# Kernel optimization log

Hardware: AMD Instinct MI355X
Metric: run time of the kernel (lower is better)

Reference implementation:

```python
import jax, jax.numpy as jnp
import numpy as np

IN_FF = 7  # joints
MASK = np.ones(9, dtype=np.float32)  # [P(3), RPY sin/cos (6)]


def _mlp(x, params):
    # params: list of (W, b); sigmoid after every layer except the last (predict)
    h = x
    for W, b in params[:-1]:
        h = jax.nn.sigmoid(h @ W + b)
    W, b = params[-1]
    return h @ W + b


def _rpy_head(x, params):
    # FeedForwardNet_RPY forward: y -> [sin(y0), cos(y1)], angle = atan2(sin, cos)
    y = _mlp(x, params)
    s = jnp.sin(y[..., 0])
    c = jnp.cos(y[..., 1])
    ang = jnp.arctan2(s, c)
    return jnp.stack([s, c, ang], axis=-1)  # (..., 3)


def setup_inputs():
    key = jax.random.key(0)
    ks = jax.random.split(key, 26)
    m = 16384
    d = {"x": jax.random.normal(ks[0], (m, 2 * IN_FF), jnp.float32)}

    def lin(k, fi, fo, name, i):
        k1, k2 = jax.random.split(k)
        lim = 1.0 / np.sqrt(fi)  # torch Linear default init
        d[name + "_W" + str(i)] = jax.random.uniform(k1, (fi, fo), jnp.float32, -lim, lim)
        d[name + "_b" + str(i)] = jax.random.uniform(k2, (fo,), jnp.float32, -lim, lim)

    idx = 1
    for name, dims in [("pos", [7, 512, 512, 3]), ("roll", [7, 256, 256, 2]),
                       ("pitch", [7, 256, 256, 2]), ("yaw", [7, 256, 256, 2])]:
        for i in range(3):
            lin(ks[idx], dims[i], dims[i + 1], name, i)
            idx += 1
    return d


def _forward(x, pos_p, roll_p, pitch_p, yaw_p):
    mask = jnp.asarray(MASK)
    M_P, M_RPY = mask[:3], mask[3:]
    q, qdot = x[:, :IN_FF], x[:, IN_FF:]

    # position net: forward + per-sample Jacobian (exact, replaces the autograd loop)
    P = _mlp(q, pos_p)                                          # (m, 3)
    J_P = jax.vmap(jax.jacfwd(lambda z: _mlp(z, pos_p)))(q)     # (m, 3, 7)
    vel = jnp.einsum("moi,mi->mo", J_P, qdot)                   # bmm(J_P, jointVels)
    P = P * M_P
    vel = vel * M_P

    heads = []
    for p in (roll_p, pitch_p, yaw_p):
        f = lambda z, p=p: _rpy_head(z, p)
        y = f(q)                                # (m, 3): [sin, cos, angle]
        J = jax.vmap(jax.jacfwd(f))(q)          # (m, 3, 7)
        v = jnp.einsum("moi,mi->mo", J[:, :2, :], qdot)  # (m, 2)
        heads.append((y, J, v))
    (yR, JR, vR), (yPi, JPi, vPi), (yY, JY, vY) = heads

    # order: [roll_sin, pitch_sin, yaw_sin, roll_cos, pitch_cos, yaw_cos]
    RPY = jnp.stack([yR[:, 0], yPi[:, 0], yY[:, 0], yR[:, 1], yPi[:, 1], yY[:, 1]], axis=1) * M_RPY
    vel_RPY = jnp.stack([vR[:, 0], vPi[:, 0], vY[:, 0], vR[:, 1], vPi[:, 1], vY[:, 1]], axis=1) * M_RPY
    J_RPY = jnp.stack([JR[:, 0], JPi[:, 0], JY[:, 0], JR[:, 1], JPi[:, 1], JY[:, 1]], axis=1)  # (m,6,7)

    out = jnp.concatenate([P, RPY, vel, vel_RPY], axis=1)            # (m, 18)
    J_tot = jnp.concatenate([J_P, J_RPY], axis=1)                    # (m, 9, 7)
    out_angles = jnp.concatenate([P, yR[:, 2:3], yPi[:, 2:3], yY[:, 2:3]], axis=1)       # (m, 6)
    J_tot_angles = jnp.concatenate([J_P, JR[:, 2:3], JPi[:, 2:3], JY[:, 2:3]], axis=1)   # (m, 6, 7)
    return out, J_tot, out_angles, J_tot_angles


def reference(x, pos_W0, pos_b0, pos_W1, pos_b1, pos_W2, pos_b2,
              roll_W0, roll_b0, roll_W1, roll_b1, roll_W2, roll_b2,
              pitch_W0, pitch_b0, pitch_W1, pitch_b1, pitch_W2, pitch_b2,
              yaw_W0, yaw_b0, yaw_W1, yaw_b1, yaw_W2, yaw_b2):
    pos_p = [(pos_W0, pos_b0), (pos_W1, pos_b1), (pos_W2, pos_b2)]
    roll_p = [(roll_W0, roll_b0), (roll_W1, roll_b1), (roll_W2, roll_b2)]
    pitch_p = [(pitch_W0, pitch_b0), (pitch_W1, pitch_b1), (pitch_W2, pitch_b2)]
    yaw_p = [(yaw_W0, yaw_b0), (yaw_W1, yaw_b1), (yaw_W2, yaw_b2)]
    return _forward(x, pos_p, roll_p, pitch_p, yaw_p)
```

## Files before the change

kernel.cpp:

```cpp
#include <hip/hip_runtime.h>
#include <math.h>

typedef __attribute__((ext_vector_type(8))) short short8;
typedef __attribute__((ext_vector_type(4))) float floatx4;

__device__ __forceinline__ float sig(float z) { return 1.0f / (1.0f + __expf(-z)); }

__device__ __forceinline__ unsigned short f2bf(float f) {
    unsigned u = __float_as_uint(f);
    u = (u + 0x7FFFu + ((u >> 16) & 1u)) >> 16;
    return (unsigned short)u;
}

__global__ void convert_w1(const float* __restrict__ src, unsigned short* __restrict__ dst,
                           int H, int logH) {
    int idx = blockIdx.x * 256 + threadIdx.x;
    if (idx >= H * H) return;
    int n = idx & (H - 1), k = idx >> logH;
    int KT = H >> 5;
    int blk = (n >> 4) * KT + (k >> 5);
    int lane = ((k >> 3) & 3) * 16 + (n & 15);
    int j = k & 7;
    dst[(blk * 64 + lane) * 8 + j] = f2bf(src[idx]);
}

struct PosS {
    float B0[512], B1[512], W2[1536];
    float Q[8][8], Qd[8][8];
    float Acc[4][64][3], Sum[64][3];
};
struct RpyS {
    float B0[256], B1[256], W2[512];
    float Q[16][8], Qd[16][8];
    float Acc[4][128][2], Sum[128][2];
};

__global__ __launch_bounds__(256, 2)
void fused_mfma(const float* __restrict__ x,
                const float* __restrict__ pW0, const float* __restrict__ pb0,
                const float* __restrict__ pb1,
                const float* __restrict__ pW2, const float* __restrict__ pb2,
                const float* __restrict__ rW0_, const float* __restrict__ rb0_,
                const float* __restrict__ rb1_,
                const float* __restrict__ rW2_, const float* __restrict__ rb2_,
                const float* __restrict__ piW0, const float* __restrict__ pib0,
                const float* __restrict__ pib1,
                const float* __restrict__ piW2, const float* __restrict__ pib2,
                const float* __restrict__ yW0, const float* __restrict__ yb0,
                const float* __restrict__ yb1,
                const float* __restrict__ yW2, const float* __restrict__ yb2,
                const unsigned short* __restrict__ wsBase,
                float* __restrict__ out, int ns)
{
    extern __shared__ unsigned short sA[];
    __shared__ union { PosS p; RpyS r; } sU;

    const int tid = threadIdx.x;
    const int f = blockIdx.x;
    const int g = f / 5, r5 = f % 5;
    const size_t JTOT = (size_t)ns * 18, OUTA = (size_t)ns * 81, JANG = (size_t)ns * 87;
    const floatx4 z4 = {0.f, 0.f, 0.f, 0.f};
    const int w = tid >> 6, lane = tid & 63;
    const int quad = lane >> 4, col = lane & 15;
    const int srcl = lane & 47;

    if (r5 < 2) {
        const int m0 = (g * 2 + r5) * 8;
        const unsigned short* wsW1 = wsBase;

        for (int i = tid; i < 512;  i += 256) { sU.p.B0[i] = pb0[i]; sU.p.B1[i] = pb1[i]; }
        for (int i = tid; i < 1536; i += 256) sU.p.W2[i] = pW2[i];
        if (tid < 112) {
            int m = tid / 14, c = tid % 14;
            float v = x[(m0 + m) * 14 + c];
            if (c < 7) sU.p.Q[m][c] = v; else sU.p.Qd[m][c - 7] = v;
        }
        __syncthreads();

        const float4* W04 = (const float4*)pW0;
        #pragma unroll
        for (int t = 0; t < 2; ++t) {
            int item = tid + t * 256;
            int s = item >> 6, k8 = item & 63;
            float q[7], w0v[7][8];
            #pragma unroll
            for (int i = 0; i < 7; i++) {
                q[i] = sU.p.Q[s][i];
                float4 a = W04[i * 128 + k8 * 2], b4 = W04[i * 128 + k8 * 2 + 1];
                w0v[i][0]=a.x; w0v[i][1]=a.y; w0v[i][2]=a.z; w0v[i][3]=a.w;
                w0v[i][4]=b4.x; w0v[i][5]=b4.y; w0v[i][6]=b4.z; w0v[i][7]=b4.w;
            }
            float hv[8], dv[8];
            #pragma unroll
            for (int jj = 0; jj < 8; jj++) {
                float z = sU.p.B0[k8 * 8 + jj];
                #pragma unroll
                for (int i = 0; i < 7; i++) z = fmaf(q[i], w0v[i][jj], z);
                float h = sig(z);
                hv[jj] = h; dv[jj] = h - h * h;
            }
            int kt = k8 >> 2, kq = k8 & 3, sw = kt & 7;
            int rr0 = s * 8;
            {
                short8 v;
                #pragma unroll
                for (int jj = 0; jj < 8; jj++) v[jj] = (short)f2bf(hv[jj]);
                *(short8*)&sA[((rr0 >> 4) * 16 + kt) * 512 + ((kq * 16 + (rr0 & 15)) ^ sw) * 8] = v;
            }
            #pragma unroll
            for (int i = 0; i < 7; i++) {
                int rr = rr0 + 1 + i;
                short8 v;
                #pragma unroll
                for (int jj = 0; jj < 8; jj++) v[jj] = (short)f2bf(dv[jj] * w0v[i][jj]);
                *(short8*)&sA[((rr >> 4) * 16 + kt) * 512 + ((kq * 16 + (rr & 15)) ^ sw) * 8] = v;
            }
        }
        __syncthreads();

        floatx4 acc[4][8];
        #pragma unroll
        for (int rt = 0; rt < 4; rt++)
            #pragma unroll
            for (int ct = 0; ct < 8; ct++) acc[rt][ct] = z4;

        const short8* bbase = (const short8*)wsW1 + (size_t)(w * 8 * 16) * 64 + lane;
        short8 bufA[8], bufB[8];
        #pragma unroll
        for (int ct = 0; ct < 8; ++ct) bufA[ct] = bbase[(ct * 16) * 64];

        for (int kt2 = 0; kt2 < 16; kt2 += 2) {
            #pragma unroll
            for (int ct = 0; ct < 8; ++ct) bufB[ct] = bbase[(ct * 16 + kt2 + 1) * 64];
            {
                const int kt = kt2, sw = kt & 7;
                short8 afr[4];
                #pragma unroll
                for (int rt = 0; rt < 4; ++rt)
                    afr[rt] = *(const short8*)&sA[(rt * 16 + kt) * 512 + (lane ^ sw) * 8];
                #pragma unroll
                for (int ct = 0; ct < 8; ++ct)
                    #pragma unroll
                    for (int rt = 0; rt < 4; ++rt)
                        acc[rt][ct] = __builtin_amdgcn_mfma_f32_16x16x32_bf16(afr[rt], bufA[ct], acc[rt][ct], 0, 0, 0);
            }
            if (kt2 + 2 < 16) {
                #pragma unroll
                for (int ct = 0; ct < 8; ++ct) bufA[ct] = bbase[(ct * 16 + kt2 + 2) * 64];
            }
            {
                const int kt = kt2 + 1, sw = kt & 7;
                short8 afr[4];
                #pragma unroll
                for (int rt = 0; rt < 4; ++rt)
                    afr[rt] = *(const short8*)&sA[(rt * 16 + kt) * 512 + (lane ^ sw) * 8];
                #pragma unroll
                for (int ct = 0; ct < 8; ++ct)
                    #pragma unroll
                    for (int rt = 0; rt < 4; ++rt)
                        acc[rt][ct] = __builtin_amdgcn_mfma_f32_16x16x32_bf16(afr[rt], bufB[ct], acc[rt][ct], 0, 0, 0);
            }
        }

        float ep[4][4][3];
        #pragma unroll
        for (int a = 0; a < 4; a++) for (int b = 0; b < 4; b++) for (int c = 0; c < 3; c++) ep[a][b][c] = 0.f;

        #pragma unroll
        for (int ct = 0; ct < 8; ++ct) {
            const int n = w * 128 + ct * 16 + col;
            const float b1n = sU.p.B1[n];
            const float w20 = sU.p.W2[n * 3], w21 = sU.p.W2[n * 3 + 1], w22 = sU.p.W2[n * 3 + 2];
            #pragma unroll
            for (int rt = 0; rt < 4; ++rt) {
                float z2c = __shfl(acc[rt][ct][0], srcl);
                float h2 = sig(z2c + b1n);
                float d2 = h2 - h2 * h2;
                #pragma unroll
                for (int r = 0; r < 4; ++r) {
                    float gg = ((quad & 1) == 0 && r == 0) ? h2 : d2 * acc[rt][ct][r];
                    ep[rt][r][0] = fmaf(gg, w20, ep[rt][r][0]);
                    ep[rt][r][1] = fmaf(gg, w21, ep[rt][r][1]);
                    ep[rt][r][2] = fmaf(gg, w22, ep[rt][r][2]);
                }
            }
        }

        #pragma unroll
        for (int mask = 1; mask <= 8; mask <<= 1)
            #pragma unroll
            for (int a = 0; a < 4; a++)
                #pragma unroll
                for (int b = 0; b < 4; b++)
                    #pragma unroll
                    for (int c = 0; c < 3; c++)
                        ep[a][b][c] += __shfl_xor(ep[a][b][c], mask);
        if (col == 0) {
            #pragma unroll
            for (int rt = 0; rt < 4; ++rt)
                #pragma unroll
                for (int r = 0; r < 4; ++r) {
                    int row = rt * 16 + quad * 4 + r;
                    sU.p.Acc[w][row][0] = ep[rt][r][0];
                    sU.p.Acc[w][row][1] = ep[rt][r][1];
                    sU.p.Acc[w][row][2] = ep[rt][r][2];
                }
        }
        __syncthreads();

        if (tid < 192) {
            int row = tid / 3, j = tid % 3;
            float v = sU.p.Acc[0][row][j] + sU.p.Acc[1][row][j] + sU.p.Acc[2][row][j] + sU.p.Acc[3][row][j];
            int s = row >> 3, i = row & 7;
            size_t M = m0 + s;
            if (i == 0) { v += pb2[j]; out[M * 18 + j] = v; out[OUTA + M * 6 + j] = v; }
            else        { out[JTOT + M * 63 + j * 7 + (i - 1)] = v;
                          out[JANG + M * 42 + j * 7 + (i - 1)] = v; }
            sU.p.Sum[row][j] = v;
        }
        __syncthreads();
        if (tid < 24) {
            int s = tid / 3, j = tid % 3;
            float vel = 0.f;
            #pragma unroll
            for (int i = 0; i < 7; i++) vel = fmaf(sU.p.Sum[s * 8 + 1 + i][j], sU.p.Qd[s][i], vel);
            out[(size_t)(m0 + s) * 18 + 9 + j] = vel;
        }
    } else {
        const int h = r5 - 2;
        const int m0 = g * 16;
        const float* W0 = (h == 0) ? rW0_ : (h == 1) ? piW0 : yW0;
        const float* b0 = (h == 0) ? rb0_ : (h == 1) ? pib0 : yb0;
        const float* b1 = (h == 0) ? rb1_ : (h == 1) ? pib1 : yb1;
        const float* W2 = (h == 0) ? rW2_ : (h == 1) ? piW2 : yW2;
        const float* b2 = (h == 0) ? rb2_ : (h == 1) ? pib2 : yb2;
        const unsigned short* wsW1 = wsBase + 262144 + h * 65536;

        if (tid < 256) { sU.r.B0[tid] = b0[tid]; sU.r.B1[tid] = b1[tid]; }
        for (int i = tid; i < 512; i += 256) sU.r.W2[i] = W2[i];
        if (tid < 224) {
            int m = tid / 14, c = tid % 14;
            float v = x[(m0 + m) * 14 + c];
            if (c < 7) sU.r.Q[m][c] = v; else sU.r.Qd[m][c - 7] = v;
        }
        __syncthreads();

        const float4* W04 = (const float4*)W0;
        #pragma unroll
        for (int t = 0; t < 2; ++t) {
            int item = tid + t * 256;
            int s = item >> 5, k8 = item & 31;
            float q[7], w0v[7][8];
            #pragma unroll
            for (int i = 0; i < 7; i++) {
                q[i] = sU.r.Q[s][i];
                float4 a = W04[i * 64 + k8 * 2], b4 = W04[i * 64 + k8 * 2 + 1];
                w0v[i][0]=a.x; w0v[i][1]=a.y; w0v[i][2]=a.z; w0v[i][3]=a.w;
                w0v[i][4]=b4.x; w0v[i][5]=b4.y; w0v[i][6]=b4.z; w0v[i][7]=b4.w;
            }
            float hv[8], dv[8];
            #pragma unroll
            for (int jj = 0; jj < 8; jj++) {
                float z = sU.r.B0[k8 * 8 + jj];
                #pragma unroll
                for (int i = 0; i < 7; i++) z = fmaf(q[i], w0v[i][jj], z);
                float hh = sig(z);
                hv[jj] = hh; dv[jj] = hh - hh * hh;
            }
            int kt = k8 >> 2, kq = k8 & 3, sw = kt & 7;
            int rr0 = s * 8;
            {
                short8 v;
                #pragma unroll
                for (int jj = 0; jj < 8; jj++) v[jj] = (short)f2bf(hv[jj]);
                *(short8*)&sA[((rr0 >> 4) * 8 + kt) * 512 + ((kq * 16 + (rr0 & 15)) ^ sw) * 8] = v;
            }
            #pragma unroll
            for (int i = 0; i < 7; i++) {
                int rr = rr0 + 1 + i;
                short8 v;
                #pragma unroll
                for (int jj = 0; jj < 8; jj++) v[jj] = (short)f2bf(dv[jj] * w0v[i][jj]);
                *(short8*)&sA[((rr >> 4) * 8 + kt) * 512 + ((kq * 16 + (rr & 15)) ^ sw) * 8] = v;
            }
        }
        __syncthreads();

        floatx4 acc[8][4];
        #pragma unroll
        for (int rt = 0; rt < 8; rt++)
            #pragma unroll
            for (int ct = 0; ct < 4; ct++) acc[rt][ct] = z4;

        const short8* bbase = (const short8*)wsW1 + (size_t)(w * 4 * 8) * 64 + lane;
        short8 bufA[4], bufB[4];
        #pragma unroll
        for (int ct = 0; ct < 4; ++ct) bufA[ct] = bbase[(ct * 8) * 64];

        for (int kt2 = 0; kt2 < 8; kt2 += 2) {
            #pragma unroll
            for (int ct = 0; ct < 4; ++ct) bufB[ct] = bbase[(ct * 8 + kt2 + 1) * 64];
            {
                const int kt = kt2, sw = kt & 7;
                short8 afr[8];
                #pragma unroll
                for (int rt = 0; rt < 8; ++rt)
                    afr[rt] = *(const short8*)&sA[(rt * 8 + kt) * 512 + (lane ^ sw) * 8];
                #pragma unroll
                for (int ct = 0; ct < 4; ++ct)
                    #pragma unroll
                    for (int rt = 0; rt < 8; ++rt)
                        acc[rt][ct] = __builtin_amdgcn_mfma_f32_16x16x32_bf16(afr[rt], bufA[ct], acc[rt][ct], 0, 0, 0);
            }
            if (kt2 + 2 < 8) {
                #pragma unroll
                for (int ct = 0; ct < 4; ++ct) bufA[ct] = bbase[(ct * 8 + kt2 + 2) * 64];
            }
            {
                const int kt = kt2 + 1, sw = kt & 7;
                short8 afr[8];
                #pragma unroll
                for (int rt = 0; rt < 8; ++rt)
                    afr[rt] = *(const short8*)&sA[(rt * 8 + kt) * 512 + (lane ^ sw) * 8];
                #pragma unroll
                for (int ct = 0; ct < 4; ++ct)
                    #pragma unroll
                    for (int rt = 0; rt < 8; ++rt)
                        acc[rt][ct] = __builtin_amdgcn_mfma_f32_16x16x32_bf16(afr[rt], bufB[ct], acc[rt][ct], 0, 0, 0);
            }
        }

        float ep[8][4][2];
        #pragma unroll
        for (int a = 0; a < 8; a++) for (int b = 0; b < 4; b++) for (int c = 0; c < 2; c++) ep[a][b][c] = 0.f;

        #pragma unroll
        for (int ct = 0; ct < 4; ++ct) {
            const int n = w * 64 + ct * 16 + col;
            const float b1n = sU.r.B1[n];
            const float w20 = sU.r.W2[n * 2], w21 = sU.r.W2[n * 2 + 1];
            #pragma unroll
            for (int rt = 0; rt < 8; ++rt) {
                float z2c = __shfl(acc[rt][ct][0], srcl);
                float h2 = sig(z2c + b1n);
                float d2 = h2 - h2 * h2;
                #pragma unroll
                for (int r = 0; r < 4; ++r) {
                    float gg = ((quad & 1) == 0 && r == 0) ? h2 : d2 * acc[rt][ct][r];
                    ep[rt][r][0] = fmaf(gg, w20, ep[rt][r][0]);
                    ep[rt][r][1] = fmaf(gg, w21, ep[rt][r][1]);
                }
            }
        }

        #pragma unroll
        for (int mask = 1; mask <= 8; mask <<= 1)
            #pragma unroll
            for (int a = 0; a < 8; a++)
                #pragma unroll
                for (int b = 0; b < 4; b++)
                    #pragma unroll
                    for (int c = 0; c < 2; c++)
                        ep[a][b][c] += __shfl_xor(ep[a][b][c], mask);
        if (col == 0) {
            #pragma unroll
            for (int rt = 0; rt < 8; ++rt)
                #pragma unroll
                for (int r = 0; r < 4; ++r) {
                    int row = rt * 16 + quad * 4 + r;
                    sU.r.Acc[w][row][0] = ep[rt][r][0];
                    sU.r.Acc[w][row][1] = ep[rt][r][1];
                }
        }
        __syncthreads();

        if (tid < 256) {
            int row = tid >> 1, j = tid & 1;
            float v = sU.r.Acc[0][row][j] + sU.r.Acc[1][row][j] + sU.r.Acc[2][row][j] + sU.r.Acc[3][row][j];
            if ((row & 7) == 0) v += b2[j];
            sU.r.Sum[row][j] = v;
        }
        __syncthreads();

        if (tid < 16) {
            int s = tid;
            size_t M = m0 + s;
            float y0 = sU.r.Sum[s * 8][0], y1 = sU.r.Sum[s * 8][1];
            float sv = sinf(y0), cv = cosf(y1);
            out[M * 18 + 3 + h] = sv;
            out[M * 18 + 6 + h] = cv;
            out[OUTA + M * 6 + 3 + h] = atan2f(sv, cv);
            float f0 = cosf(y0), f1 = -sinf(y1);
            float inv = 1.0f / fmaf(sv, sv, cv * cv);
            float v0 = 0.f, v1 = 0.f;
            #pragma unroll
            for (int i = 0; i < 7; i++) {
                float r0 = f0 * sU.r.Sum[s * 8 + 1 + i][0];
                float r1 = f1 * sU.r.Sum[s * 8 + 1 + i][1];
                out[JTOT + M * 63 + (3 + h) * 7 + i] = r0;
                out[JTOT + M * 63 + (6 + h) * 7 + i] = r1;
                out[JANG + M * 42 + (3 + h) * 7 + i] = (cv * r0 - sv * r1) * inv;
                v0 = fmaf(r0, sU.r.Qd[s][i], v0);
                v1 = fmaf(r1, sU.r.Qd[s][i], v1);
            }
            out[M * 18 + 12 + h] = v0;
            out[M * 18 + 15 + h] = v1;
        }
    }
}

extern "C" void kernel_launch(void* const* d_in, const int* in_sizes, int n_in,
                              void* d_out, int out_size, void* d_ws, size_t ws_size,
                              hipStream_t stream) {
    (void)n_in; (void)out_size; (void)ws_size;
    const float* x = (const float*)d_in[0];
    float* out = (float*)d_out;
    unsigned short* ws = (unsigned short*)d_ws;
    const int ns = in_sizes[0] / 14;

    convert_w1<<<dim3((512 * 512) / 256), 256, 0, stream>>>((const float*)d_in[3],  ws,          512, 9);
    convert_w1<<<dim3((256 * 256) / 256), 256, 0, stream>>>((const float*)d_in[9],  ws + 262144, 256, 8);
    convert_w1<<<dim3((256 * 256) / 256), 256, 0, stream>>>((const float*)d_in[15], ws + 327680, 256, 8);
    convert_w1<<<dim3((256 * 256) / 256), 256, 0, stream>>>((const float*)d_in[21], ws + 393216, 256, 8);

    fused_mfma<<<dim3((ns / 8 / 2) * 5), 256, 65536, stream>>>(
        x,
        (const float*)d_in[1],  (const float*)d_in[2],  (const float*)d_in[4],
        (const float*)d_in[5],  (const float*)d_in[6],
        (const float*)d_in[7],  (const float*)d_in[8],  (const float*)d_in[10],
        (const float*)d_in[11], (const float*)d_in[12],
        (const float*)d_in[13], (const float*)d_in[14], (const float*)d_in[16],
        (const float*)d_in[17], (const float*)d_in[18],
        (const float*)d_in[19], (const float*)d_in[20], (const float*)d_in[22],
        (const float*)d_in[23], (const float*)d_in[24],
        ws, out, ns);
}
```

Measured before the change: 335.9 us.

## Halve samples per block, raise occupancy, merge weight conversion launches

Each block now handles half as many samples (4 for pos, 8 for RPY), so the grid doubles and dynamic LDS shrinks to 32 KB. The per-wave accumulator tiles shrink, and launch bounds rise to 3 blocks per CU. The reduction scratch moves into the reused dynamic LDS, and the double-buffered B prefetch becomes a simple unrolled loop. The four weight conversion kernels are merged into one launch, and the layer-1 staging writes packed bf16 pairs. The trade is more blocks each reloading biases, W2 and W1 tiles from global memory, which roughly doubles weight traffic per sample.

```diff
diff --git a/kernel.cpp b/kernel.cpp
--- a/kernel.cpp
+++ b/kernel.cpp
@@ -12,30 +12,37 @@
     return (unsigned short)u;
 }
 
-__global__ void convert_w1(const float* __restrict__ src, unsigned short* __restrict__ dst,
-                           int H, int logH) {
+__device__ __forceinline__ unsigned int pack2bf(float a, float b) {
+    unsigned ua = __float_as_uint(a), ub = __float_as_uint(b);
+    ua += 0x7FFFu + ((ua >> 16) & 1u);
+    ub += 0x7FFFu + ((ub >> 16) & 1u);
+    return __builtin_amdgcn_perm(ub, ua, 0x07060302);
+}
+
+__global__ void convert_all(const float* __restrict__ s0, const float* __restrict__ s1,
+                            const float* __restrict__ s2, const float* __restrict__ s3,
+                            unsigned short* __restrict__ ws) {
     int idx = blockIdx.x * 256 + threadIdx.x;
-    if (idx >= H * H) return;
-    int n = idx & (H - 1), k = idx >> logH;
+    const float* src; unsigned short* dst; int H, logH, local;
+    if (idx < 262144) { src = s0; dst = ws; H = 512; logH = 9; local = idx; }
+    else {
+        int r = idx - 262144; int m = r >> 16; local = r & 65535;
+        H = 256; logH = 8;
+        src = (m == 0) ? s1 : (m == 1) ? s2 : s3;
+        dst = ws + 262144 + m * 65536;
+    }
+    int n = local & (H - 1), k = local >> logH;
     int KT = H >> 5;
     int blk = (n >> 4) * KT + (k >> 5);
     int lane = ((k >> 3) & 3) * 16 + (n & 15);
     int j = k & 7;
-    dst[(blk * 64 + lane) * 8 + j] = f2bf(src[idx]);
-}
-
-struct PosS {
-    float B0[512], B1[512], W2[1536];
-    float Q[8][8], Qd[8][8];
-    float Acc[4][64][3], Sum[64][3];
-};
-struct RpyS {
-    float B0[256], B1[256], W2[512];
-    float Q[16][8], Qd[16][8];
-    float Acc[4][128][2], Sum[128][2];
-};
-
-__global__ __launch_bounds__(256, 2)
+    dst[(blk * 64 + lane) * 8 + j] = f2bf(src[local]);
+}
+
+struct PosS { float B0[512], B1[512], W2[1536], Q[4][8], Qd[4][8]; };
+struct RpyS { float B0[256], B1[256], W2[512],  Q[8][8], Qd[8][8]; };
+
+__global__ __launch_bounds__(256, 3)
 void fused_mfma(const float* __restrict__ x,
                 const float* __restrict__ pW0, const float* __restrict__ pb0,
                 const float* __restrict__ pb1,
@@ -53,6 +60,7 @@
                 float* __restrict__ out, int ns)
 {
     extern __shared__ unsigned short sA[];
+    float* dynF = (float*)sA;
     __shared__ union { PosS p; RpyS r; } sU;
 
     const int tid = threadIdx.x;
@@ -65,12 +73,11 @@
     const int srcl = lane & 47;
 
     if (r5 < 2) {
-        const int m0 = (g * 2 + r5) * 8;
-        const unsigned short* wsW1 = wsBase;
+        const int m0 = (g * 2 + r5) * 4;
 
         for (int i = tid; i < 512;  i += 256) { sU.p.B0[i] = pb0[i]; sU.p.B1[i] = pb1[i]; }
         for (int i = tid; i < 1536; i += 256) sU.p.W2[i] = pW2[i];
-        if (tid < 112) {
+        if (tid < 56) {
             int m = tid / 14, c = tid % 14;
             float v = x[(m0 + m) * 14 + c];
             if (c < 7) sU.p.Q[m][c] = v; else sU.p.Qd[m][c - 7] = v;
@@ -81,98 +88,71 @@
         #pragma unroll
         for (int t = 0; t < 2; ++t) {
             int item = tid + t * 256;
-            int s = item >> 6, k8 = item & 63;
-            float q[7], w0v[7][8];
+            int s = item >> 7, gg = item & 127;
+            int kt = gg >> 3, kq = (gg >> 1) & 3, j0 = (gg & 1) * 4;
+            int sw = kt & 7;
+            int k = gg * 4;
+            float q[7]; float4 w0r[7];
+            #pragma unroll
+            for (int i = 0; i < 7; i++) { q[i] = sU.p.Q[s][i]; w0r[i] = W04[i * 128 + gg]; }
+            float hv[4], dv[4];
+            #pragma unroll
+            for (int jj = 0; jj < 4; jj++) {
+                float z = sU.p.B0[k + jj];
+                #pragma unroll
+                for (int i = 0; i < 7; i++) z = fmaf(q[i], ((const float*)&w0r[i])[jj], z);
+                float hh = sig(z);
+                hv[jj] = hh; dv[jj] = hh - hh * hh;
+            }
+            const int rt = s >> 1, rb = (s & 1) * 8;
+            {
+                int cl = (kq * 16 + rb) ^ sw;
+                uint2 v; v.x = pack2bf(hv[0], hv[1]); v.y = pack2bf(hv[2], hv[3]);
+                *(uint2*)&sA[(rt * 16 + kt) * 512 + cl * 8 + j0] = v;
+            }
             #pragma unroll
             for (int i = 0; i < 7; i++) {
-                q[i] = sU.p.Q[s][i];
-                float4 a = W04[i * 128 + k8 * 2], b4 = W04[i * 128 + k8 * 2 + 1];
-                w0v[i][0]=a.x; w0v[i][1]=a.y; w0v[i][2]=a.z; w0v[i][3]=a.w;
-                w0v[i][4]=b4.x; w0v[i][5]=b4.y; w0v[i][6]=b4.z; w0v[i][7]=b4.w;
-            }
-            float hv[8], dv[8];
-            #pragma unroll
-            for (int jj = 0; jj < 8; jj++) {
-                float z = sU.p.B0[k8 * 8 + jj];
-                #pragma unroll
-                for (int i = 0; i < 7; i++) z = fmaf(q[i], w0v[i][jj], z);
-                float h = sig(z);
-                hv[jj] = h; dv[jj] = h - h * h;
-            }
-            int kt = k8 >> 2, kq = k8 & 3, sw = kt & 7;
-            int rr0 = s * 8;
-            {
-                short8 v;
-                #pragma unroll
-                for (int jj = 0; jj < 8; jj++) v[jj] = (short)f2bf(hv[jj]);
-                *(short8*)&sA[((rr0 >> 4) * 16 + kt) * 512 + ((kq * 16 + (rr0 & 15)) ^ sw) * 8] = v;
-            }
-            #pragma unroll
-            for (int i = 0; i < 7; i++) {
-                int rr = rr0 + 1 + i;
-                short8 v;
-                #pragma unroll
-                for (int jj = 0; jj < 8; jj++) v[jj] = (short)f2bf(dv[jj] * w0v[i][jj]);
-                *(short8*)&sA[((rr >> 4) * 16 + kt) * 512 + ((kq * 16 + (rr & 15)) ^ sw) * 8] = v;
-            }
-        }
-        __syncthreads();
-
-        floatx4 acc[4][8];
-        #pragma unroll
-        for (int rt = 0; rt < 4; rt++)
+                int cl = (kq * 16 + rb + 1 + i) ^ sw;
+                uint2 v;
+                v.x = pack2bf(dv[0] * ((const float*)&w0r[i])[0], dv[1] * ((const float*)&w0r[i])[1]);
+                v.y = pack2bf(dv[2] * ((const float*)&w0r[i])[2], dv[3] * ((const float*)&w0r[i])[3]);
+                *(uint2*)&sA[(rt * 16 + kt) * 512 + cl * 8 + j0] = v;
+            }
+        }
+        __syncthreads();
+
+        floatx4 acc[2][8];
+        #pragma unroll
+        for (int rt = 0; rt < 2; rt++)
             #pragma unroll
             for (int ct = 0; ct < 8; ct++) acc[rt][ct] = z4;
 
-        const short8* bbase = (const short8*)wsW1 + (size_t)(w * 8 * 16) * 64 + lane;
-        short8 bufA[8], bufB[8];
-        #pragma unroll
-        for (int ct = 0; ct < 8; ++ct) bufA[ct] = bbase[(ct * 16) * 64];
-
-        for (int kt2 = 0; kt2 < 16; kt2 += 2) {
-            #pragma unroll
-            for (int ct = 0; ct < 8; ++ct) bufB[ct] = bbase[(ct * 16 + kt2 + 1) * 64];
-            {
-                const int kt = kt2, sw = kt & 7;
-                short8 afr[4];
-                #pragma unroll
-                for (int rt = 0; rt < 4; ++rt)
-                    afr[rt] = *(const short8*)&sA[(rt * 16 + kt) * 512 + (lane ^ sw) * 8];
-                #pragma unroll
-                for (int ct = 0; ct < 8; ++ct)
-                    #pragma unroll
-                    for (int rt = 0; rt < 4; ++rt)
-                        acc[rt][ct] = __builtin_amdgcn_mfma_f32_16x16x32_bf16(afr[rt], bufA[ct], acc[rt][ct], 0, 0, 0);
-            }
-            if (kt2 + 2 < 16) {
-                #pragma unroll
-                for (int ct = 0; ct < 8; ++ct) bufA[ct] = bbase[(ct * 16 + kt2 + 2) * 64];
-            }
-            {
-                const int kt = kt2 + 1, sw = kt & 7;
-                short8 afr[4];
-                #pragma unroll
-                for (int rt = 0; rt < 4; ++rt)
-                    afr[rt] = *(const short8*)&sA[(rt * 16 + kt) * 512 + (lane ^ sw) * 8];
-                #pragma unroll
-                for (int ct = 0; ct < 8; ++ct)
-                    #pragma unroll
-                    for (int rt = 0; rt < 4; ++rt)
-                        acc[rt][ct] = __builtin_amdgcn_mfma_f32_16x16x32_bf16(afr[rt], bufB[ct], acc[rt][ct], 0, 0, 0);
-            }
-        }
-
-        float ep[4][4][3];
-        #pragma unroll
-        for (int a = 0; a < 4; a++) for (int b = 0; b < 4; b++) for (int c = 0; c < 3; c++) ep[a][b][c] = 0.f;
-
+        const short8* bbase = (const short8*)wsBase + (size_t)(w * 128) * 64 + lane;
+        #pragma unroll
+        for (int kt = 0; kt < 16; ++kt) {
+            const int sw = kt & 7;
+            short8 bf[8];
+            #pragma unroll
+            for (int ct = 0; ct < 8; ++ct) bf[ct] = bbase[(ct * 16 + kt) * 64];
+            short8 a0 = *(const short8*)&sA[(kt) * 512 + (lane ^ sw) * 8];
+            short8 a1 = *(const short8*)&sA[(16 + kt) * 512 + (lane ^ sw) * 8];
+            #pragma unroll
+            for (int ct = 0; ct < 8; ++ct) {
+                acc[0][ct] = __builtin_amdgcn_mfma_f32_16x16x32_bf16(a0, bf[ct], acc[0][ct], 0, 0, 0);
+                acc[1][ct] = __builtin_amdgcn_mfma_f32_16x16x32_bf16(a1, bf[ct], acc[1][ct], 0, 0, 0);
+            }
+        }
+
+        float ep[2][4][3];
+        #pragma unroll
+        for (int a = 0; a < 2; a++) for (int b = 0; b < 4; b++) for (int c = 0; c < 3; c++) ep[a][b][c] = 0.f;
         #pragma unroll
         for (int ct = 0; ct < 8; ++ct) {
             const int n = w * 128 + ct * 16 + col;
             const float b1n = sU.p.B1[n];
             const float w20 = sU.p.W2[n * 3], w21 = sU.p.W2[n * 3 + 1], w22 = sU.p.W2[n * 3 + 2];
             #pragma unroll
-            for (int rt = 0; rt < 4; ++rt) {
+            for (int rt = 0; rt < 2; ++rt) {
                 float z2c = __shfl(acc[rt][ct][0], srcl);
                 float h2 = sig(z2c + b1n);
                 float d2 = h2 - h2 * h2;
@@ -185,50 +165,51 @@
                 }
             }
         }
-
         #pragma unroll
         for (int mask = 1; mask <= 8; mask <<= 1)
             #pragma unroll
-            for (int a = 0; a < 4; a++)
+            for (int a = 0; a < 2; a++)
                 #pragma unroll
                 for (int b = 0; b < 4; b++)
                     #pragma unroll
                     for (int c = 0; c < 3; c++)
                         ep[a][b][c] += __shfl_xor(ep[a][b][c], mask);
+        __syncthreads();
         if (col == 0) {
             #pragma unroll
-            for (int rt = 0; rt < 4; ++rt)
+            for (int rt = 0; rt < 2; ++rt)
                 #pragma unroll
                 for (int r = 0; r < 4; ++r) {
                     int row = rt * 16 + quad * 4 + r;
-                    sU.p.Acc[w][row][0] = ep[rt][r][0];
-                    sU.p.Acc[w][row][1] = ep[rt][r][1];
-                    sU.p.Acc[w][row][2] = ep[rt][r][2];
+                    dynF[(w * 32 + row) * 3 + 0] = ep[rt][r][0];
+                    dynF[(w * 32 + row) * 3 + 1] = ep[rt][r][1];
+                    dynF[(w * 32 + row) * 3 + 2] = ep[rt][r][2];
                 }
         }
         __syncthreads();
-
-        if (tid < 192) {
+        if (tid < 96) {
             int row = tid / 3, j = tid % 3;
-            float v = sU.p.Acc[0][row][j] + sU.p.Acc[1][row][j] + sU.p.Acc[2][row][j] + sU.p.Acc[3][row][j];
-            int s = row >> 3, i = row & 7;
+            float v = dynF[row * 3 + j] + dynF[(32 + row) * 3 + j]
+                    + dynF[(64 + row) * 3 + j] + dynF[(96 + row) * 3 + j];
+            int i_row = row & 7, s = row >> 3;
             size_t M = m0 + s;
-            if (i == 0) { v += pb2[j]; out[M * 18 + j] = v; out[OUTA + M * 6 + j] = v; }
-            else        { out[JTOT + M * 63 + j * 7 + (i - 1)] = v;
-                          out[JANG + M * 42 + j * 7 + (i - 1)] = v; }
-            sU.p.Sum[row][j] = v;
-        }
-        __syncthreads();
-        if (tid < 24) {
+            if (i_row == 0) { v += pb2[j]; out[M * 18 + j] = v; out[OUTA + M * 6 + j] = v; }
+            else            { out[JTOT + M * 63 + j * 7 + (i_row - 1)] = v;
+                              out[JANG + M * 42 + j * 7 + (i_row - 1)] = v; }
+            dynF[384 + row * 3 + j] = v;
+        }
+        __syncthreads();
+        if (tid < 12) {
             int s = tid / 3, j = tid % 3;
             float vel = 0.f;
             #pragma unroll
-            for (int i = 0; i < 7; i++) vel = fmaf(sU.p.Sum[s * 8 + 1 + i][j], sU.p.Qd[s][i], vel);
+            for (int i = 0; i < 7; i++)
+                vel = fmaf(dynF[384 + (s * 8 + 1 + i) * 3 + j], sU.p.Qd[s][i], vel);
             out[(size_t)(m0 + s) * 18 + 9 + j] = vel;
         }
     } else {
         const int h = r5 - 2;
-        const int m0 = g * 16;
+        const int m0 = g * 8;
         const float* W0 = (h == 0) ? rW0_ : (h == 1) ? piW0 : yW0;
         const float* b0 = (h == 0) ? rb0_ : (h == 1) ? pib0 : yb0;
         const float* b1 = (h == 0) ? rb1_ : (h == 1) ? pib1 : yb1;
@@ -238,7 +219,7 @@
 
         if (tid < 256) { sU.r.B0[tid] = b0[tid]; sU.r.B1[tid] = b1[tid]; }
         for (int i = tid; i < 512; i += 256) sU.r.W2[i] = W2[i];
-        if (tid < 224) {
+        if (tid < 112) {
             int m = tid / 14, c = tid % 14;
             float v = x[(m0 + m) * 14 + c];
             if (c < 7) sU.r.Q[m][c] = v; else sU.r.Qd[m][c - 7] = v;
@@ -249,98 +230,73 @@
         #pragma unroll
         for (int t = 0; t < 2; ++t) {
             int item = tid + t * 256;
-            int s = item >> 5, k8 = item & 31;
-            float q[7], w0v[7][8];
-            #pragma unroll
-            for (int i = 0; i < 7; i++) {
-                q[i] = sU.r.Q[s][i];
-                float4 a = W04[i * 64 + k8 * 2], b4 = W04[i * 64 + k8 * 2 + 1];
-                w0v[i][0]=a.x; w0v[i][1]=a.y; w0v[i][2]=a.z; w0v[i][3]=a.w;
-                w0v[i][4]=b4.x; w0v[i][5]=b4.y; w0v[i][6]=b4.z; w0v[i][7]=b4.w;
-            }
-            float hv[8], dv[8];
-            #pragma unroll
-            for (int jj = 0; jj < 8; jj++) {
-                float z = sU.r.B0[k8 * 8 + jj];
-                #pragma unroll
-                for (int i = 0; i < 7; i++) z = fmaf(q[i], w0v[i][jj], z);
+            int s = item >> 6, gg = item & 63;
+            int kt = gg >> 3, kq = (gg >> 1) & 3, j0 = (gg & 1) * 4;
+            int sw = kt & 7;
+            int k = gg * 4;
+            float q[7]; float4 w0r[7];
+            #pragma unroll
+            for (int i = 0; i < 7; i++) { q[i] = sU.r.Q[s][i]; w0r[i] = W04[i * 64 + gg]; }
+            float hv[4], dv[4];
+            #pragma unroll
+            for (int jj = 0; jj < 4; jj++) {
+                float z = sU.r.B0[k + jj];
+                #pragma unroll
+                for (int i = 0; i < 7; i++) z = fmaf(q[i], ((const float*)&w0r[i])[jj], z);
                 float hh = sig(z);
                 hv[jj] = hh; dv[jj] = hh - hh * hh;
             }
-            int kt = k8 >> 2, kq = k8 & 3, sw = kt & 7;
-            int rr0 = s * 8;
+            const int rt = s >> 1, rb = (s & 1) * 8;
             {
-                short8 v;
-                #pragma unroll
-                for (int jj = 0; jj < 8; jj++) v[jj] = (short)f2bf(hv[jj]);
-                *(short8*)&sA[((rr0 >> 4) * 8 + kt) * 512 + ((kq * 16 + (rr0 & 15)) ^ sw) * 8] = v;
+                int cl = (kq * 16 + rb) ^ sw;
+                uint2 v; v.x = pack2bf(hv[0], hv[1]); v.y = pack2bf(hv[2], hv[3]);
+                *(uint2*)&sA[(rt * 8 + kt) * 512 + cl * 8 + j0] = v;
             }
             #pragma unroll
             for (int i = 0; i < 7; i++) {
-                int rr = rr0 + 1 + i;
-                short8 v;
-                #pragma unroll
-                for (int jj = 0; jj < 8; jj++) v[jj] = (short)f2bf(dv[jj] * w0v[i][jj]);
-                *(short8*)&sA[((rr >> 4) * 8 + kt) * 512 + ((kq * 16 + (rr & 15)) ^ sw) * 8] = v;
-            }
-        }
-        __syncthreads();
-
-        floatx4 acc[8][4];
-        #pragma unroll
-        for (int rt = 0; rt < 8; rt++)
+                int cl = (kq * 16 + rb + 1 + i) ^ sw;
+                uint2 v;
+                v.x = pack2bf(dv[0] * ((const float*)&w0r[i])[0], dv[1] * ((const float*)&w0r[i])[1]);
+                v.y = pack2bf(dv[2] * ((const float*)&w0r[i])[2], dv[3] * ((const float*)&w0r[i])[3]);
+                *(uint2*)&sA[(rt * 8 + kt) * 512 + cl * 8 + j0] = v;
+            }
+        }
+        __syncthreads();
+
+        floatx4 acc[4][4];
+        #pragma unroll
+        for (int rt = 0; rt < 4; rt++)
             #pragma unroll
             for (int ct = 0; ct < 4; ct++) acc[rt][ct] = z4;
 
-        const short8* bbase = (const short8*)wsW1 + (size_t)(w * 4 * 8) * 64 + lane;
-        short8 bufA[4], bufB[4];
-        #pragma unroll
-        for (int ct = 0; ct < 4; ++ct) bufA[ct] = bbase[(ct * 8) * 64];
-
-        for (int kt2 = 0; kt2 < 8; kt2 += 2) {
-            #pragma unroll
-            for (int ct = 0; ct < 4; ++ct) bufB[ct] = bbase[(ct * 8 + kt2 + 1) * 64];
-            {
-                const int kt = kt2, sw = kt & 7;
-                short8 afr[8];
-                #pragma unroll
-                for (int rt = 0; rt < 8; ++rt)
-                    afr[rt] = *(const short8*)&sA[(rt * 8 + kt) * 512 + (lane ^ sw) * 8];
-                #pragma unroll
-                for (int ct = 0; ct < 4; ++ct)
-                    #pragma unroll
-                    for (int rt = 0; rt < 8; ++rt)
-                        acc[rt][ct] = __builtin_amdgcn_mfma_f32_16x16x32_bf16(afr[rt], bufA[ct], acc[rt][ct], 0, 0, 0);
-            }
-            if (kt2 + 2 < 8) {
-                #pragma unroll
-                for (int ct = 0; ct < 4; ++ct) bufA[ct] = bbase[(ct * 8 + kt2 + 2) * 64];
-            }
-            {
-                const int kt = kt2 + 1, sw = kt & 7;
-                short8 afr[8];
-                #pragma unroll
-                for (int rt = 0; rt < 8; ++rt)
-                    afr[rt] = *(const short8*)&sA[(rt * 8 + kt) * 512 + (lane ^ sw) * 8];
-                #pragma unroll
-                for (int ct = 0; ct < 4; ++ct)
-                    #pragma unroll
-                    for (int rt = 0; rt < 8; ++rt)
-                        acc[rt][ct] = __builtin_amdgcn_mfma_f32_16x16x32_bf16(afr[rt], bufB[ct], acc[rt][ct], 0, 0, 0);
-            }
-        }
-
-        float ep[8][4][2];
-        #pragma unroll
-        for (int a = 0; a < 8; a++) for (int b = 0; b < 4; b++) for (int c = 0; c < 2; c++) ep[a][b][c] = 0.f;
-
+        const short8* bbase = (const short8*)wsW1 + (size_t)(w * 32) * 64 + lane;
+        #pragma unroll
+        for (int kt = 0; kt < 8; ++kt) {
+            const int sw = kt & 7;
+            short8 bf[4];
+            #pragma unroll
+            for (int ct = 0; ct < 4; ++ct) bf[ct] = bbase[(ct * 8 + kt) * 64];
+            short8 afr[4];
+            #pragma unroll
+            for (int rt = 0; rt < 4; ++rt)
+                afr[rt] = *(const short8*)&sA[(rt * 8 + kt) * 512 + (lane ^ sw) * 8];
+            #pragma unroll
+            for (int ct = 0; ct < 4; ++ct)
+                #pragma unroll
+                for (int rt = 0; rt < 4; ++rt)
+                    acc[rt][ct] = __builtin_amdgcn_mfma_f32_16x16x32_bf16(afr[rt], bf[ct], acc[rt][ct], 0, 0, 0);
+        }
+
+        float ep[4][4][2];
+        #pragma unroll
+        for (int a = 0; a < 4; a++) for (int b = 0; b < 4; b++) for (int c = 0; c < 2; c++) ep[a][b][c] = 0.f;
         #pragma unroll
         for (int ct = 0; ct < 4; ++ct) {
             const int n = w * 64 + ct * 16 + col;
             const float b1n = sU.r.B1[n];
             const float w20 = sU.r.W2[n * 2], w21 = sU.r.W2[n * 2 + 1];
             #pragma unroll
-            for (int rt = 0; rt < 8; ++rt) {
+            for (int rt = 0; rt < 4; ++rt) {
                 float z2c = __shfl(acc[rt][ct][0], srcl);
                 float h2 = sig(z2c + b1n);
                 float d2 = h2 - h2 * h2;
@@ -352,40 +308,39 @@
                 }
             }
         }
-
         #pragma unroll
         for (int mask = 1; mask <= 8; mask <<= 1)
             #pragma unroll
-            for (int a = 0; a < 8; a++)
+            for (int a = 0; a < 4; a++)
                 #pragma unroll
                 for (int b = 0; b < 4; b++)
                     #pragma unroll
                     for (int c = 0; c < 2; c++)
                         ep[a][b][c] += __shfl_xor(ep[a][b][c], mask);
+        __syncthreads();
         if (col == 0) {
             #pragma unroll
-            for (int rt = 0; rt < 8; ++rt)
+            for (int rt = 0; rt < 4; ++rt)
                 #pragma unroll
                 for (int r = 0; r < 4; ++r) {
                     int row = rt * 16 + quad * 4 + r;
-                    sU.r.Acc[w][row][0] = ep[rt][r][0];
-                    sU.r.Acc[w][row][1] = ep[rt][r][1];
+                    dynF[(w * 64 + row) * 2 + 0] = ep[rt][r][0];
+                    dynF[(w * 64 + row) * 2 + 1] = ep[rt][r][1];
                 }
         }
         __syncthreads();
-
-        if (tid < 256) {
+        if (tid < 128) {
             int row = tid >> 1, j = tid & 1;
-            float v = sU.r.Acc[0][row][j] + sU.r.Acc[1][row][j] + sU.r.Acc[2][row][j] + sU.r.Acc[3][row][j];
+            float v = dynF[row * 2 + j] + dynF[(64 + row) * 2 + j]
+                    + dynF[(128 + row) * 2 + j] + dynF[(192 + row) * 2 + j];
             if ((row & 7) == 0) v += b2[j];
-            sU.r.Sum[row][j] = v;
-        }
-        __syncthreads();
-
-        if (tid < 16) {
+            dynF[512 + row * 2 + j] = v;
+        }
+        __syncthreads();
+        if (tid < 8) {
             int s = tid;
             size_t M = m0 + s;
-            float y0 = sU.r.Sum[s * 8][0], y1 = sU.r.Sum[s * 8][1];
+            float y0 = dynF[512 + (s * 8) * 2 + 0], y1 = dynF[512 + (s * 8) * 2 + 1];
             float sv = sinf(y0), cv = cosf(y1);
             out[M * 18 + 3 + h] = sv;
             out[M * 18 + 6 + h] = cv;
@@ -395,8 +350,8 @@
             float v0 = 0.f, v1 = 0.f;
             #pragma unroll
             for (int i = 0; i < 7; i++) {
-                float r0 = f0 * sU.r.Sum[s * 8 + 1 + i][0];
-                float r1 = f1 * sU.r.Sum[s * 8 + 1 + i][1];
+                float r0 = f0 * dynF[512 + (s * 8 + 1 + i) * 2 + 0];
+                float r1 = f1 * dynF[512 + (s * 8 + 1 + i) * 2 + 1];
                 out[JTOT + M * 63 + (3 + h) * 7 + i] = r0;
                 out[JTOT + M * 63 + (6 + h) * 7 + i] = r1;
                 out[JANG + M * 42 + (3 + h) * 7 + i] = (cv * r0 - sv * r1) * inv;
@@ -418,12 +373,11 @@
     unsigned short* ws = (unsigned short*)d_ws;
     const int ns = in_sizes[0] / 14;
 
-    convert_w1<<<dim3((512 * 512) / 256), 256, 0, stream>>>((const float*)d_in[3],  ws,          512, 9);
-    convert_w1<<<dim3((256 * 256) / 256), 256, 0, stream>>>((const float*)d_in[9],  ws + 262144, 256, 8);
-    convert_w1<<<dim3((256 * 256) / 256), 256, 0, stream>>>((const float*)d_in[15], ws + 327680, 256, 8);
-    convert_w1<<<dim3((256 * 256) / 256), 256, 0, stream>>>((const float*)d_in[21], ws + 393216, 256, 8);
-
-    fused_mfma<<<dim3((ns / 8 / 2) * 5), 256, 65536, stream>>>(
+    convert_all<<<dim3(1792), 256, 0, stream>>>(
+        (const float*)d_in[3], (const float*)d_in[9],
+        (const float*)d_in[15], (const float*)d_in[21], ws);
+
+    fused_mfma<<<dim3((ns / 8) * 5), 256, 32768, stream>>>(
         x,
         (const float*)d_in[1],  (const float*)d_in[2],  (const float*)d_in[4],
         (const float*)d_in[5],  (const float*)d_in[6],
```

Result: slower. 349.6 us (+4.1%).
